# Kernel tuning notes

Measured on AMD Instinct MI355X. Metric: run time of the kernel, lower is better.

The kernel has to match this reference:

```python
import jax, jax.numpy as jnp
import numpy as np

B, R, C, A, K = 32, 13, 13, 5, 20
CELL = K + 5                      # 4 coords + objectness + 20 classes
N = R * C * A                     # 845 boxes per image
THRESH = 0.5
NMS_TH = 0.4
BIAS_VALS = [1.3221, 1.73145, 3.19275, 4.00944, 5.05587,
             8.09892, 9.47112, 4.84053, 11.2364, 10.0071]


def setup_inputs() -> dict:
    key = jax.random.key(0)
    x = jax.random.normal(key, (B, R, C, A * CELL), dtype=jnp.float32)
    bias = jnp.array(BIAS_VALS, dtype=jnp.float32)  # anchor priors (w,h interleaved)
    return {"x": x, "bias": bias}


def _nms_keep(iou, scores):
    """Greedy per-class NMS. iou: [B,N,N]; scores: [B,K,N] (already thresholded).
    Returns bool keep mask [B,K,N]. Decisions are non-differentiable, so inputs
    are stop_gradient'ed by the caller."""
    Bn = scores.shape[0]
    valid = scores > THRESH
    order = jnp.argsort(-scores, axis=-1)          # descending score order [B,K,N]
    rank = jnp.argsort(order, axis=-1)             # inverse permutation   [B,K,N]
    barange = jnp.arange(Bn)[:, None]

    def body(i, suppressed):
        idx = order[:, :, i]                                              # [B,K]
        sup_i = jnp.take_along_axis(suppressed, idx[:, :, None], -1)[..., 0]
        val_i = jnp.take_along_axis(valid, idx[:, :, None], -1)[..., 0]
        alive = val_i & ~sup_i                                            # [B,K]
        row = iou[barange, idx]                                           # [B,K,N]
        return suppressed | (alive[..., None] & (row > NMS_TH) & (rank > i))

    suppressed = jax.lax.fori_loop(0, N, body, jnp.zeros((Bn, K, N), bool))
    return valid & ~suppressed


def reference(x, bias):
    Bn, R_, C_, _ = x.shape
    t = x.reshape(Bn, R_, C_, A, CELL)
    gx = jnp.arange(C_, dtype=x.dtype)
    gy = jnp.arange(R_, dtype=x.dtype)
    # box decode (matches source: hNorm=rows used for width, wNorm=cols for height)
    bx = (jax.nn.sigmoid(t[..., 0]) + gx[None, None, :, None]) / C_
    by = (jax.nn.sigmoid(t[..., 1]) + gy[None, :, None, None]) / R_
    bw = jnp.exp(t[..., 2]) * bias[0::2] / R_
    bh = jnp.exp(t[..., 3]) * bias[1::2] / C_
    obj = jax.nn.sigmoid(t[..., 4])
    cls = jax.nn.softmax(t[..., 5:], axis=-1)
    prob = obj[..., None] * cls
    prob = jnp.where(prob > THRESH, prob, 0.0)

    # flatten to box index layout (y*cols + x)*anchors + a, same as source
    flat = lambda a: a.reshape(Bn, N)
    bx, by, bw, bh, obj = map(flat, (bx, by, bw, bh, obj))
    prob = prob.reshape(Bn, N, K)

    # corner-form boxes for IoU (source uses x - w/2, y - h/2, w, h)
    x1 = bx - bw * 0.5
    y1 = by - bh * 0.5
    x2 = x1 + bw
    y2 = y1 + bh
    iw = jnp.maximum(0.0, jnp.minimum(x2[:, :, None], x2[:, None, :]) -
                          jnp.maximum(x1[:, :, None], x1[:, None, :]))
    ih = jnp.maximum(0.0, jnp.minimum(y2[:, :, None], y2[:, None, :]) -
                          jnp.maximum(y1[:, :, None], y1[:, None, :]))
    inter = iw * ih
    area = bw * bh
    union = area[:, :, None] + area[:, None, :] - inter
    iou = inter / jnp.maximum(union, 1e-9)                       # [B,N,N]

    scores = prob.transpose(0, 2, 1)                             # [B,K,N]
    keep = _nms_keep(jax.lax.stop_gradient(iou),
                     jax.lax.stop_gradient(scores))
    out_prob = jnp.where(keep, scores, 0.0).transpose(0, 2, 1)   # [B,N,K]

    out = jnp.concatenate([bx[..., None], by[..., None], bw[..., None],
                           bh[..., None], obj[..., None], out_prob], axis=-1)
    return out  # [B, N, CELL]
```

## Files before the change

kernel.cpp:

```cpp
#include <hip/hip_runtime.h>
#include <math.h>

#define BN 32
#define RR 13
#define CC 13
#define AA 5
#define KK 20
#define CELLSZ 25
#define NN (RR * CC * AA)
#define THRESH 0.5f
#define NMS_TH 0.4f
#define NT 256

__device__ __forceinline__ float sigmoidf_(float x) {
    return 1.0f / (1.0f + expf(-x));
}

__global__ __launch_bounds__(NT) void region_fused_kernel(
        const float* __restrict__ x,
        const float* __restrict__ bias,
        float* __restrict__ out) {
    __shared__ float sx1[NN], sy1[NN], sx2[NN], sy2[NN], sar[NN], ssc[NN];
    __shared__ unsigned char st[NN];
    __shared__ float red_s[NT];
    __shared__ int   red_i[NT];

    const int b   = blockIdx.x / KK;
    const int k   = blockIdx.x % KK;
    const int tid = threadIdx.x;

    for (int n = tid; n < NN; n += NT) {
        int r   = n / (CC * AA);
        int rem = n % (CC * AA);
        int c   = rem / AA;
        int a   = rem % AA;
        const float* t = x + (((size_t)(b * RR + r) * CC + c) * AA + a) * CELLSZ;

        float bx  = (sigmoidf_(t[0]) + (float)c) / (float)CC;
        float by  = (sigmoidf_(t[1]) + (float)r) / (float)RR;
        float bw  = expf(t[2]) * bias[2 * a]     / (float)RR;
        float bh  = expf(t[3]) * bias[2 * a + 1] / (float)CC;
        float obj = sigmoidf_(t[4]);

        float m = t[5];
#pragma unroll
        for (int j = 1; j < KK; ++j) m = fmaxf(m, t[5 + j]);
        float s = 0.0f;
#pragma unroll
        for (int j = 0; j < KK; ++j) s += expf(t[5 + j] - m);
        float sck = obj * (expf(t[5 + k] - m) / s);

        float x1 = bx - bw * 0.5f;
        float y1 = by - bh * 0.5f;
        sx1[n] = x1;
        sy1[n] = y1;
        sx2[n] = x1 + bw;
        sy2[n] = y1 + bh;
        sar[n] = bw * bh;
        ssc[n] = sck;
        st[n]  = (sck > THRESH) ? 0 : 1;

        if (k == 0) {
            float* o = out + (size_t)(b * NN + n) * CELLSZ;
            o[0] = bx; o[1] = by; o[2] = bw; o[3] = bh; o[4] = obj;
        }
    }
    __syncthreads();

    while (true) {
        float best = -1.0f;
        int   bi   = 0x7fffffff;
        for (int n = tid; n < NN; n += NT) {
            if (st[n] == 0) {
                float sc = ssc[n];
                if (sc > best) { best = sc; bi = n; }
            }
        }
        red_s[tid] = best;
        red_i[tid] = bi;
        __syncthreads();
        if (tid < 64) {
            float s0 = red_s[tid];
            int   i0 = red_i[tid];
#pragma unroll
            for (int off = 64; off < NT; off += 64) {
                float so = red_s[tid + off];
                int   io = red_i[tid + off];
                if (so > s0 || (so == s0 && io < i0)) { s0 = so; i0 = io; }
            }
#pragma unroll
            for (int off = 32; off > 0; off >>= 1) {
                float so = __shfl_down(s0, off);
                int   io = __shfl_down(i0, off);
                if (so > s0 || (so == s0 && io < i0)) { s0 = so; i0 = io; }
            }
            if (tid == 0) { red_s[0] = s0; red_i[0] = i0; }
        }
        __syncthreads();
        float bsc = red_s[0];
        int   sel = red_i[0];

        if (bsc < 0.0f) break;

        if (tid == 0) st[sel] = 2;

        float X1 = sx1[sel], Y1 = sy1[sel], X2 = sx2[sel], Y2 = sy2[sel];
        float AR = sar[sel];
        for (int n = tid; n < NN; n += NT) {
            if (n != sel && st[n] == 0) {
                float iw = fmaxf(0.0f, fminf(X2, sx2[n]) - fmaxf(X1, sx1[n]));
                float ih = fmaxf(0.0f, fminf(Y2, sy2[n]) - fmaxf(Y1, sy1[n]));
                float inter = iw * ih;
                float uni   = AR + sar[n] - inter;
                float iou   = inter / fmaxf(uni, 1e-9f);
                if (iou > NMS_TH) st[n] = 1;
            }
        }
        __syncthreads();
    }

    for (int n = tid; n < NN; n += NT) {
        out[(size_t)(b * NN + n) * CELLSZ + 5 + k] = (st[n] == 2) ? ssc[n] : 0.0f;
    }
}

extern "C" void kernel_launch(void* const* d_in, const int* in_sizes, int n_in,
                              void* d_out, int out_size, void* d_ws, size_t ws_size,
                              hipStream_t stream) {
    const float* x    = (const float*)d_in[0];
    const float* bias = (const float*)d_in[1];
    float* out = (float*)d_out;

    region_fused_kernel<<<BN * KK, NT, 0, stream>>>(x, bias, out);
}
```

Baseline: 72.72 us.

## Split into decode kernel with candidate compaction and single-wavefront NMS over candidates

Replaces the fused per-(batch,class) block, which decoded all 845 boxes 20 times, with a decode kernel that computes each box once, writes the output, and appends above-threshold (batch,class) candidates to a global list via atomics. A second kernel runs greedy NMS with one 64-lane wavefront per (batch,class), iterating only over the compacted candidates, using alive bitmasks and shuffle reductions instead of block-wide syncs. This removes redundant decode work and the barrier-heavy loop over all boxes. In exchange it adds a memset and an extra launch, relies on workspace layout and atomics, and uses a 32-bit alive mask that caps candidates at 2048.

```diff
diff --git a/kernel.cpp b/kernel.cpp
--- a/kernel.cpp
+++ b/kernel.cpp
@@ -8,119 +8,144 @@
 #define KK 20
 #define CELLSZ 25
 #define NN (RR * CC * AA)
+#define NBK (BN * KK)
 #define THRESH 0.5f
 #define NMS_TH 0.4f
-#define NT 256
+
+#define CAND_OFF 4096
+#define REC 8
+#define CAP NN
 
 __device__ __forceinline__ float sigmoidf_(float x) {
     return 1.0f / (1.0f + expf(-x));
 }
 
-__global__ __launch_bounds__(NT) void region_fused_kernel(
+__global__ __launch_bounds__(256) void decode_kernel(
         const float* __restrict__ x,
         const float* __restrict__ bias,
-        float* __restrict__ out) {
-    __shared__ float sx1[NN], sy1[NN], sx2[NN], sy2[NN], sar[NN], ssc[NN];
-    __shared__ unsigned char st[NN];
-    __shared__ float red_s[NT];
-    __shared__ int   red_i[NT];
+        float* __restrict__ out,
+        int* __restrict__ cnt,
+        float* __restrict__ cand) {
+    int idx = blockIdx.x * 256 + threadIdx.x;
+    if (idx >= BN * NN) return;
+    int b   = idx / NN;
+    int n   = idx % NN;
+    int r   = n / (CC * AA);
+    int rem = n % (CC * AA);
+    int c   = rem / AA;
+    int a   = rem % AA;
 
-    const int b   = blockIdx.x / KK;
-    const int k   = blockIdx.x % KK;
-    const int tid = threadIdx.x;
+    const float* t = x + (size_t)idx * CELLSZ;
 
-    for (int n = tid; n < NN; n += NT) {
-        int r   = n / (CC * AA);
-        int rem = n % (CC * AA);
-        int c   = rem / AA;
-        int a   = rem % AA;
-        const float* t = x + (((size_t)(b * RR + r) * CC + c) * AA + a) * CELLSZ;
+    float bx  = (sigmoidf_(t[0]) + (float)c) / (float)CC;
+    float by  = (sigmoidf_(t[1]) + (float)r) / (float)RR;
+    float bw  = expf(t[2]) * bias[2 * a]     / (float)RR;
+    float bh  = expf(t[3]) * bias[2 * a + 1] / (float)CC;
+    float obj = sigmoidf_(t[4]);
 
-        float bx  = (sigmoidf_(t[0]) + (float)c) / (float)CC;
-        float by  = (sigmoidf_(t[1]) + (float)r) / (float)RR;
-        float bw  = expf(t[2]) * bias[2 * a]     / (float)RR;
-        float bh  = expf(t[3]) * bias[2 * a + 1] / (float)CC;
-        float obj = sigmoidf_(t[4]);
+    float l[KK];
+    float m = t[5];
+#pragma unroll
+    for (int k = 0; k < KK; ++k) { l[k] = t[5 + k]; m = fmaxf(m, l[k]); }
+    float s = 0.0f;
+#pragma unroll
+    for (int k = 0; k < KK; ++k) { l[k] = expf(l[k] - m); s += l[k]; }
 
-        float m = t[5];
+    float* o = out + (size_t)idx * CELLSZ;
+    o[0] = bx; o[1] = by; o[2] = bw; o[3] = bh; o[4] = obj;
 #pragma unroll
-        for (int j = 1; j < KK; ++j) m = fmaxf(m, t[5 + j]);
-        float s = 0.0f;
+    for (int k = 0; k < KK; ++k) o[5 + k] = 0.0f;
+
 #pragma unroll
-        for (int j = 0; j < KK; ++j) s += expf(t[5 + j] - m);
-        float sck = obj * (expf(t[5 + k] - m) / s);
-
-        float x1 = bx - bw * 0.5f;
-        float y1 = by - bh * 0.5f;
-        sx1[n] = x1;
-        sy1[n] = y1;
-        sx2[n] = x1 + bw;
-        sy2[n] = y1 + bh;
-        sar[n] = bw * bh;
-        ssc[n] = sck;
-        st[n]  = (sck > THRESH) ? 0 : 1;
-
-        if (k == 0) {
-            float* o = out + (size_t)(b * NN + n) * CELLSZ;
-            o[0] = bx; o[1] = by; o[2] = bw; o[3] = bh; o[4] = obj;
+    for (int k = 0; k < KK; ++k) {
+        float p = obj * (l[k] / s);
+        if (p > THRESH) {
+            int bk   = b * KK + k;
+            int slot = atomicAdd(&cnt[bk], 1);
+            float* rec = cand + ((size_t)bk * CAP + slot) * REC;
+            float x1 = bx - bw * 0.5f;
+            float y1 = by - bh * 0.5f;
+            rec[0] = __int_as_float(n);
+            rec[1] = p;
+            rec[2] = x1;
+            rec[3] = y1;
+            rec[4] = x1 + bw;
+            rec[5] = y1 + bh;
+            rec[6] = bw * bh;
         }
     }
-    __syncthreads();
+}
+
+__global__ __launch_bounds__(64) void nms_kernel(
+        const int* __restrict__ cnt,
+        const float* __restrict__ cand,
+        float* __restrict__ out) {
+    int bk = blockIdx.x;
+    int m  = cnt[bk];
+    if (m <= 0) return;
+    int b    = bk / KK;
+    int k    = bk % KK;
+    int lane = threadIdx.x;
+    const float* list = cand + (size_t)bk * CAP * REC;
+
+    if (m == 1) {
+        if (lane == 0) {
+            int n = __float_as_int(list[0]);
+            out[((size_t)b * NN + n) * CELLSZ + 5 + k] = list[1];
+        }
+        return;
+    }
+
+    int T = (m + 63) >> 6;
+    unsigned alive = 0;
+    for (int tt = 0; tt < T; ++tt) {
+        int j = lane + (tt << 6);
+        if (j < m) alive |= 1u << tt;
+    }
 
     while (true) {
-        float best = -1.0f;
-        int   bi   = 0x7fffffff;
-        for (int n = tid; n < NN; n += NT) {
-            if (st[n] == 0) {
-                float sc = ssc[n];
-                if (sc > best) { best = sc; bi = n; }
+        float bs = -1.0f;
+        int   bn = 0x7fffffff;
+        int   bg = -1;
+        for (int tt = 0; tt < T; ++tt) {
+            if ((alive >> tt) & 1u) {
+                int j = lane + (tt << 6);
+                float sc = list[j * REC + 1];
+                int   nn = __float_as_int(list[j * REC]);
+                if (sc > bs || (sc == bs && nn < bn)) { bs = sc; bn = nn; bg = j; }
             }
         }
-        red_s[tid] = best;
-        red_i[tid] = bi;
-        __syncthreads();
-        if (tid < 64) {
-            float s0 = red_s[tid];
-            int   i0 = red_i[tid];
 #pragma unroll
-            for (int off = 64; off < NT; off += 64) {
-                float so = red_s[tid + off];
-                int   io = red_i[tid + off];
-                if (so > s0 || (so == s0 && io < i0)) { s0 = so; i0 = io; }
-            }
-#pragma unroll
-            for (int off = 32; off > 0; off >>= 1) {
-                float so = __shfl_down(s0, off);
-                int   io = __shfl_down(i0, off);
-                if (so > s0 || (so == s0 && io < i0)) { s0 = so; i0 = io; }
-            }
-            if (tid == 0) { red_s[0] = s0; red_i[0] = i0; }
+        for (int off = 32; off > 0; off >>= 1) {
+            float os = __shfl_xor(bs, off);
+            int   on = __shfl_xor(bn, off);
+            int   og = __shfl_xor(bg, off);
+            if (os > bs || (os == bs && on < bn)) { bs = os; bn = on; bg = og; }
         }
-        __syncthreads();
-        float bsc = red_s[0];
-        int   sel = red_i[0];
+        if (bg < 0) break;
 
-        if (bsc < 0.0f) break;
+        float X1 = list[bg * REC + 2];
+        float Y1 = list[bg * REC + 3];
+        float X2 = list[bg * REC + 4];
+        float Y2 = list[bg * REC + 5];
+        float AR = list[bg * REC + 6];
 
-        if (tid == 0) st[sel] = 2;
+        if ((bg & 63) == lane) {
+            out[((size_t)b * NN + bn) * CELLSZ + 5 + k] = bs;
+            alive &= ~(1u << (bg >> 6));
+        }
 
-        float X1 = sx1[sel], Y1 = sy1[sel], X2 = sx2[sel], Y2 = sy2[sel];
-        float AR = sar[sel];
-        for (int n = tid; n < NN; n += NT) {
-            if (n != sel && st[n] == 0) {
-                float iw = fmaxf(0.0f, fminf(X2, sx2[n]) - fmaxf(X1, sx1[n]));
-                float ih = fmaxf(0.0f, fminf(Y2, sy2[n]) - fmaxf(Y1, sy1[n]));
+        for (int tt = 0; tt < T; ++tt) {
+            int j = lane + (tt << 6);
+            if (((alive >> tt) & 1u) && j != bg) {
+                float iw = fmaxf(0.0f, fminf(X2, list[j * REC + 4]) - fmaxf(X1, list[j * REC + 2]));
+                float ih = fmaxf(0.0f, fminf(Y2, list[j * REC + 5]) - fmaxf(Y1, list[j * REC + 3]));
                 float inter = iw * ih;
-                float uni   = AR + sar[n] - inter;
+                float uni   = AR + list[j * REC + 6] - inter;
                 float iou   = inter / fmaxf(uni, 1e-9f);
-                if (iou > NMS_TH) st[n] = 1;
+                if (iou > NMS_TH) alive &= ~(1u << tt);
             }
         }
-        __syncthreads();
-    }
-
-    for (int n = tid; n < NN; n += NT) {
-        out[(size_t)(b * NN + n) * CELLSZ + 5 + k] = (st[n] == 2) ? ssc[n] : 0.0f;
     }
 }
 
@@ -131,5 +156,10 @@
     const float* bias = (const float*)d_in[1];
     float* out = (float*)d_out;
 
-    region_fused_kernel<<<BN * KK, NT, 0, stream>>>(x, bias, out);
+    int*   cnt  = (int*)d_ws;
+    float* cand = (float*)((char*)d_ws + CAND_OFF);
+
+    hipMemsetAsync(cnt, 0, NBK * sizeof(int), stream);
+    decode_kernel<<<(BN * NN + 255) / 256, 256, 0, stream>>>(x, bias, out, cnt, cand);
+    nms_kernel<<<NBK, 64, 0, stream>>>(cnt, cand, out);
 }
```

New measurement: 62.59 us. 13.9% less time.
